# Optimization experiments

Hardware: AMD Instinct MI355X
Metric: run time of the kernel (lower is better)

The kernel has to match this reference:

```python
import jax, jax.numpy as jnp
import numpy as np
from jax import lax

NUM_CLASSES = 102
IN_CAPS = 2592
IN_DIM = 8
OUT_DIM = 16
ROUTINGS = 3
IMG = 112

def squash(s, axis=-1, eps=1e-8):
    sq = jnp.sum(s * s, axis=axis, keepdims=True)
    return (sq / (1.0 + sq)) * s / jnp.sqrt(sq + eps)

def conv2d(x, w, b, stride):
    y = lax.conv_general_dilated(x, w, (stride, stride), 'VALID',
                                 dimension_numbers=('NCHW', 'OIHW', 'NCHW'))
    return y + b[None, :, None, None]

def setup_inputs() -> dict:
    key = jax.random.key(0)
    ks = jax.random.split(key, 12)
    B = 32
    x = jax.random.normal(ks[0], (B, 3, IMG, IMG), jnp.float32)
    targets = jax.random.randint(ks[1], (B,), 0, NUM_CLASSES)
    conv1_w = jax.random.normal(ks[2], (256, 3, 11, 11), jnp.float32) * 0.02
    conv1_b = jnp.zeros((256,), jnp.float32)
    pc_w = jax.random.normal(ks[3], (256, 256, 9, 9), jnp.float32) * 0.02
    pc_b = jnp.zeros((256,), jnp.float32)
    W = jax.random.normal(ks[4], (NUM_CLASSES, IN_CAPS, OUT_DIM, IN_DIM), jnp.float32) * 0.01
    fc1_w = jax.random.normal(ks[5], (NUM_CLASSES * OUT_DIM, 512), jnp.float32) * 0.02
    fc1_b = jnp.zeros((512,), jnp.float32)
    fc2_w = jax.random.normal(ks[6], (512, 1024), jnp.float32) * 0.02
    fc2_b = jnp.zeros((1024,), jnp.float32)
    fc3_w = jax.random.normal(ks[7], (1024, 3 * IMG * IMG), jnp.float32) * 0.02
    fc3_b = jnp.zeros((3 * IMG * IMG,), jnp.float32)
    return dict(x=x, targets=targets, conv1_w=conv1_w, conv1_b=conv1_b,
                pc_w=pc_w, pc_b=pc_b, W=W,
                fc1_w=fc1_w, fc1_b=fc1_b, fc2_w=fc2_w, fc2_b=fc2_b,
                fc3_w=fc3_w, fc3_b=fc3_b)

def reference(x, targets, conv1_w, conv1_b, pc_w, pc_b, W,
              fc1_w, fc1_b, fc2_w, fc2_b, fc3_w, fc3_b):
    B = x.shape[0]
    # conv backbone: [B,3,112,112] -> [B,256,34,34]
    feat = jax.nn.relu(conv2d(x, conv1_w, conv1_b, 3))
    # primary caps conv: -> [B,256,9,9] -> [B,2592,8], squash
    pc = conv2d(feat, pc_w, pc_b, 3)
    u = squash(pc.reshape(B, IN_CAPS, IN_DIM))
    # prediction vectors: [B, O, N, D_out]
    x_hat = jnp.einsum('ondi,bni->bond', W, u)
    x_hat_sg = lax.stop_gradient(x_hat)
    b = jnp.zeros((B, NUM_CLASSES, IN_CAPS), x.dtype)
    v = None
    for it in range(ROUTINGS):
        c = jax.nn.softmax(b, axis=1)  # couple over out caps
        xh = x_hat if it == ROUTINGS - 1 else x_hat_sg
        s = jnp.einsum('bon,bond->bod', c, xh)
        v = squash(s)
        if it < ROUTINGS - 1:
            b = b + jnp.einsum('bond,bod->bon', xh, v)
    # reconstruction: mask by target class capsule
    mask = jax.nn.one_hot(targets, NUM_CLASSES, dtype=v.dtype)
    h = (v * mask[:, :, None]).reshape(B, NUM_CLASSES * OUT_DIM)
    h = jax.nn.relu(h @ fc1_w + fc1_b)
    h = jax.nn.relu(h @ fc2_w + fc2_b)
    recon = jax.nn.sigmoid(h @ fc3_w + fc3_b).reshape(B, 3, IMG, IMG)
    return (v, recon)
```

## Files before the change

### kernel.cpp

```cpp
#include <hip/hip_runtime.h>
#include <hip/hip_fp16.h>
#include <math.h>

#define B32   32
#define OCLS  102
#define NCAPS 2592

#define OFF_FEAT   0u
#define OFF_C1WT   10027008u
#define OFF_PCWQ   10076160u
#define OFF_PCP    11780096u
#define OFF_WQ2    17088512u
#define OFF_WQ     25555456u
#define OFF_U2     34022400u
#define OFF_CT     34685952u
#define OFF_DEN    38916096u
#define OFF_S      38999040u
#define OFF_V0     39051264u
#define OFF_V1     39103488u
#define OFF_VSQ    39155712u
#define OFF_H2T    39185152u
#define OFF_FC3P   39217920u

typedef __attribute__((ext_vector_type(8))) short short8;
typedef __attribute__((ext_vector_type(4))) float f32x4;
typedef long long i64;

__device__ __forceinline__ unsigned short f2b(float f) {
  union { float f; unsigned u; } v; v.f = f;
  unsigned r = v.u + 0x7fffu + ((v.u >> 16) & 1u);
  return (unsigned short)(r >> 16);
}

__device__ __forceinline__ float b2f(unsigned short h) {
  union { unsigned u; float f; } v; v.u = ((unsigned)h) << 16;
  return v.f;
}

__device__ __forceinline__ unsigned f2q_fast(float x) {
  union { float f; unsigned u; } v; v.f = x;
  unsigned s = (v.u >> 24) & 0x80u;
  unsigned au = v.u & 0x7fffffffu;
  if (au < 0x3c800000u) return s;
  if (au >= 0x43e00000u) return s | 0x7eu;
  unsigned r = au + 0x7ffffu + ((au >> 20) & 1u);
  unsigned e = (r >> 23) - 120u;
  unsigned m = (r >> 20) & 7u;
  return s | (e << 3) | m;
}

__device__ __forceinline__ unsigned fp8pair(float a, float b) {
#if __has_builtin(__builtin_amdgcn_cvt_pk_fp8_f32)
  return (unsigned)__builtin_amdgcn_cvt_pk_fp8_f32(a, b, 0, false) & 0xffffu;
#else
  return f2q_fast(a) | (f2q_fast(b) << 8);
#endif
}

__device__ __forceinline__ float rcpf(float x) {
#if __has_builtin(__builtin_amdgcn_rcpf)
  return __builtin_amdgcn_rcpf(x);
#else
  return 1.0f / x;
#endif
}

__global__ __launch_bounds__(256) void k_pack(const float* __restrict__ conv1_w,
                                              const float* __restrict__ pc_w,
                                              const float* __restrict__ W,
                                              unsigned short* __restrict__ C1WB,
                                              unsigned char* __restrict__ PCWQ,
                                              unsigned char* __restrict__ Wq2,
                                              unsigned char* __restrict__ Wq,
                                              float* __restrict__ S) {
  __shared__ unsigned char sq[64 * 128];
  int bb = blockIdx.x;
  int t = threadIdx.x;
  if (bb < 256) {
    if (t < 128) {
#pragma unroll
      for (int ci = 0; ci < 3; ++ci) {
        float v = (t < 121) ? conv1_w[bb * 363 + ci * 121 + t] : 0.f;
        C1WB[(ci * 256 + bb) * 128 + t] = f2b(v);
      }
    }
  } else if (bb < 512) {
    int co = bb - 256;
    for (int e = t; e < 20736; e += 256) {
      int ci = e / 81, tap = e - ci * 81;
      PCWQ[(size_t)ci * 26624 + co * 104 + tap] =
          (unsigned char)f2q_fast(pc_w[(size_t)co * 20736 + e] * 64.f);
    }
    for (int tap = 81; tap < 104; ++tap)
      PCWQ[(size_t)t * 26624 + co * 104 + tap] = 0;
  } else if (bb < 4643) {
    size_t base = (size_t)(bb - 512) * 8192;
    int g = t >> 3, seg = t & 7;
    int r0 = 2 * g, r1 = 2 * g + 1;
    const f32x4* s0 = (const f32x4*)(W + base + r0 * 128 + seg * 16);
    const f32x4* s1 = (const f32x4*)(W + base + r1 * 128 + seg * 16);
    f32x4 a0 = s0[0], a1 = s0[1], a2 = s0[2], a3 = s0[3];
    f32x4 c0 = s1[0], c1 = s1[1], c2 = s1[2], c3 = s1[3];
    asm volatile("" :: "v"(a0), "v"(a1), "v"(a2), "v"(a3),
                       "v"(c0), "v"(c1), "v"(c2), "v"(c3));
    unsigned w0[4], w1[4];
    f32x4 va[4] = {a0, a1, a2, a3}, vc[4] = {c0, c1, c2, c3};
#pragma unroll
    for (int j = 0; j < 4; ++j) {
      w0[j] = fp8pair(va[j][0] * 64.f, va[j][1] * 64.f) |
              (fp8pair(va[j][2] * 64.f, va[j][3] * 64.f) << 16);
      w1[j] = fp8pair(vc[j][0] * 64.f, vc[j][1] * 64.f) |
              (fp8pair(vc[j][2] * 64.f, vc[j][3] * 64.f) << 16);
    }
    *(uint4*)(Wq2 + base + r0 * 128 + seg * 16) = make_uint4(w0[0], w0[1], w0[2], w0[3]);
    *(uint4*)(Wq2 + base + r1 * 128 + seg * 16) = make_uint4(w1[0], w1[1], w1[2], w1[3]);
#pragma unroll
    for (int e = 0; e < 16; ++e) {
      int idx = seg * 16 + e, d = idx >> 3, i = idx & 7;
      sq[r0 * 128 + i * 16 + d] = (unsigned char)((w0[e >> 2] >> ((e & 3) * 8)) & 0xffu);
      sq[r1 * 128 + i * 16 + d] = (unsigned char)((w1[e >> 2] >> ((e & 3) * 8)) & 0xffu);
    }
    __syncthreads();
    *(uint4*)(Wq + base + (size_t)t * 16) = ((const uint4*)sq)[t];
    *(uint4*)(Wq + base + 4096 + (size_t)t * 16) = ((const uint4*)sq)[256 + t];
  } else {
    int idx = (bb - 4643) * 1024 + t * 4;
    *(float4*)(S + idx) = make_float4(0.f, 0.f, 0.f, 0.f);
  }
}

__global__ __launch_bounds__(256) void k_c1m(const float* __restrict__ x,
                                             const unsigned short* __restrict__ C1WB,
                                             const float* __restrict__ bias,
                                             unsigned short* __restrict__ feat2) {
  __shared__ unsigned short sh[48 * 128 + 128 * 128];
  unsigned short* lA = sh;
  unsigned short* lB = sh + 48 * 128;
  unsigned short* obuf = sh + 48 * 128;

  int bx = blockIdx.x;
  int hf = blockIdx.y;
  int b = bx / 34, ho = bx % 34;
  int t = threadIdx.x;
  int lane = t & 63, wv = t >> 6;
  int l15 = lane & 15, lh = lane >> 4;
  int rx = l15 & 7;

  {
    uint4 zz = make_uint4(0, 0, 0, 0);
    uint4* z = (uint4*)lA;
    for (int i = t; i < 48 * 128 / 8; i += 256) z[i] = zz;
  }
  __syncthreads();

  f32x4 acc[3][2];
#pragma unroll
  for (int mf = 0; mf < 3; ++mf)
#pragma unroll
    for (int nf = 0; nf < 2; ++nf) acc[mf][nf] = (f32x4){0.f, 0.f, 0.f, 0.f};

#pragma unroll 1
  for (int ci = 0; ci < 3; ++ci) {
    {
      const uint4* Bsrc = (const uint4*)(C1WB + ci * 32768 + hf * 16384);
#pragma unroll
      for (int i = 0; i < 8; ++i) {
        int f = i * 256 + t;
        int row = f >> 4, cu = f & 15;
        ((uint4*)lB)[row * 16 + (cu ^ (row & 7))] = Bsrc[f];
      }
    }
    for (int tk = t; tk < 374; tk += 256) {
      int kh = tk / 34, wo = tk - kh * 34;
      const float* src = x + ((size_t)(b * 3 + ci) * 112 + ho * 3 + kh) * 112 + wo * 3;
#pragma unroll
      for (int j = 0; j < 11; ++j) {
        int tap = kh * 11 + j;
        int cu = tap >> 3;
        lA[wo * 128 + (((cu ^ (wo & 7)) << 3) | (tap & 7))] = f2b(src[j]);
      }
    }
    __syncthreads();

#pragma unroll
    for (int s = 0; s < 4; ++s) {
      int cub = ((s * 4 + lh) ^ rx) << 3;
      short8 a0 = *(const short8*)(lA + (0 + l15) * 128 + cub);
      short8 a1 = *(const short8*)(lA + (16 + l15) * 128 + cub);
      short8 a2 = *(const short8*)(lA + (32 + l15) * 128 + cub);
      short8 b0 = *(const short8*)(lB + (wv * 32 + 0 + l15) * 128 + cub);
      short8 b1 = *(const short8*)(lB + (wv * 32 + 16 + l15) * 128 + cub);
      acc[0][0] = __builtin_amdgcn_mfma_f32_16x16x32_bf16(a0, b0, acc[0][0], 0, 0, 0);
      acc[0][1] = __builtin_amdgcn_mfma_f32_16x16x32_bf16(a0, b1, acc[0][1], 0, 0, 0);
      acc[1][0] = __builtin_amdgcn_mfma_f32_16x16x32_bf16(a1, b0, acc[1][0], 0, 0, 0);
      acc[1][1] = __builtin_amdgcn_mfma_f32_16x16x32_bf16(a1, b1, acc[1][1], 0, 0, 0);
      acc[2][0] = __builtin_amdgcn_mfma_f32_16x16x32_bf16(a2, b0, acc[2][0], 0, 0, 0);
      acc[2][1] = __builtin_amdgcn_mfma_f32_16x16x32_bf16(a2, b1, acc[2][1], 0, 0, 0);
    }
    __syncthreads();
  }

  float bv[2];
#pragma unroll
  for (int nf = 0; nf < 2; ++nf) bv[nf] = bias[hf * 128 + wv * 32 + nf * 16 + l15];
#pragma unroll
  for (int mf = 0; mf < 3; ++mf)
#pragma unroll
    for (int nf = 0; nf < 2; ++nf)
#pragma unroll
      for (int r = 0; r < 4; ++r) {
        int wo = mf * 16 + lh * 4 + r;
        if (wo < 36)
          obuf[(wv * 32 + nf * 16 + l15) * 36 + wo] =
              f2b(fmaxf(acc[mf][nf][r] + bv[nf], 0.f));
      }
  __syncthreads();
  uint4* dst = (uint4*)(feat2 + (size_t)bx * 9216 + hf * 4608);
  const uint4* srcb = (const uint4*)obuf;
  for (int i = t; i < 576; i += 256) dst[i] = srcb[i];
}

__device__ __forceinline__ void pc_gather8(const unsigned short* __restrict__ feat2,
                                           unsigned char* __restrict__ dstbuf,
                                           int mb, int ci, int t) {
  for (int task = t; task < 576; task += 256) {
    int m = task / 9, kh = task - m * 9;
    int gm = mb * 64 + m;
    if (gm < 2592) {
      int b = gm / 81, p = gm - b * 81;
      int ho = p / 9, wo = p - ho * 9;
      const unsigned short* src =
          feat2 + ((size_t)(b * 34 + ho * 3 + kh) * 256 + ci) * 36 + wo * 3;
      unsigned char* dst = dstbuf + m * 104 + kh * 9;
      unsigned p01 = fp8pair(b2f(src[0]), b2f(src[1]));
      unsigned p23 = fp8pair(b2f(src[2]), b2f(src[3]));
      unsigned p45 = fp8pair(b2f(src[4]), b2f(src[5]));
      unsigned p67 = fp8pair(b2f(src[6]), b2f(src[7]));
      unsigned p8  = fp8pair(b2f(src[8]), 0.f);
      dst[0] = p01; dst[1] = p01 >> 8;
      dst[2] = p23; dst[3] = p23 >> 8;
      dst[4] = p45; dst[5] = p45 >> 8;
      dst[6] = p67; dst[7] = p67 >> 8;
      dst[8] = p8;
    }
  }
}

__global__ __launch_bounds__(256, 3) void k_pc4(const unsigned short* __restrict__ feat2,
                                                const unsigned char* __restrict__ PCWQ,
                                                __half* __restrict__ pcp) {
  __shared__ unsigned char lA[2][64 * 104];

  int mb = blockIdx.x, kc = blockIdx.y;
  int t = threadIdx.x;
  int lane = t & 63, wv = t >> 6;
  int l15 = lane & 15, lh = lane >> 4;

  {
    uint4 zz = make_uint4(0, 0, 0, 0);
    uint4* z = (uint4*)lA;
    for (int i = t; i < 2 * 64 * 104 / 16; i += 256) z[i] = zz;
  }
  __syncthreads();
  pc_gather8(feat2, lA[0], mb, kc * 16, t);
  __syncthreads();

  f32x4 acc[4][4];
#pragma unroll
  for (int mf = 0; mf < 4; ++mf)
#pragma unroll
    for (int nf = 0; nf < 4; ++nf) acc[mf][nf] = (f32x4){0.f, 0.f, 0.f, 0.f};

#pragma unroll 1
  for (int cil = 0; cil < 16; ++cil) {
    int ci = kc * 16 + cil;
    int cur = cil & 1;

    i64 bfr[4][3];
    const unsigned char* Bbase = PCWQ + (size_t)ci * 26624 + (wv * 64 + l15) * 104 + lh * 8;
#pragma unroll
    for (int nf = 0; nf < 4; ++nf)
#pragma unroll
      for (int s = 0; s < 3; ++s)
        bfr[nf][s] = *(const i64*)(Bbase + nf * 16 * 104 + s * 32);

    if (cil < 15) pc_gather8(feat2, lA[cur ^ 1], mb, ci + 1, t);

    const unsigned char* arow = lA[cur] + l15 * 104 + lh * 8;
#pragma unroll
    for (int s = 0; s < 3; ++s) {
      i64 a0 = *(const i64*)(arow + s * 32);
      i64 a1 = *(const i64*)(arow + 16 * 104 + s * 32);
      i64 a2 = *(const i64*)(arow + 32 * 104 + s * 32);
      i64 a3 = *(const i64*)(arow + 48 * 104 + s * 32);
      acc[0][0] = __builtin_amdgcn_mfma_f32_16x16x32_fp8_fp8(a0, bfr[0][s], acc[0][0], 0, 0, 0);
      acc[0][1] = __builtin_amdgcn_mfma_f32_16x16x32_fp8_fp8(a0, bfr[1][s], acc[0][1], 0, 0, 0);
      acc[0][2] = __builtin_amdgcn_mfma_f32_16x16x32_fp8_fp8(a0, bfr[2][s], acc[0][2], 0, 0, 0);
      acc[0][3] = __builtin_amdgcn_mfma_f32_16x16x32_fp8_fp8(a0, bfr[3][s], acc[0][3], 0, 0, 0);
      acc[1][0] = __builtin_amdgcn_mfma_f32_16x16x32_fp8_fp8(a1, bfr[0][s], acc[1][0], 0, 0, 0);
      acc[1][1] = __builtin_amdgcn_mfma_f32_16x16x32_fp8_fp8(a1, bfr[1][s], acc[1][1], 0, 0, 0);
      acc[1][2] = __builtin_amdgcn_mfma_f32_16x16x32_fp8_fp8(a1, bfr[2][s], acc[1][2], 0, 0, 0);
      acc[1][3] = __builtin_amdgcn_mfma_f32_16x16x32_fp8_fp8(a1, bfr[3][s], acc[1][3], 0, 0, 0);
      acc[2][0] = __builtin_amdgcn_mfma_f32_16x16x32_fp8_fp8(a2, bfr[0][s], acc[2][0], 0, 0, 0);
      acc[2][1] = __builtin_amdgcn_mfma_f32_16x16x32_fp8_fp8(a2, bfr[1][s], acc[2][1], 0, 0, 0);
      acc[2][2] = __builtin_amdgcn_mfma_f32_16x16x32_fp8_fp8(a2, bfr[2][s], acc[2][2], 0, 0, 0);
      acc[2][3] = __builtin_amdgcn_mfma_f32_16x16x32_fp8_fp8(a2, bfr[3][s], acc[2][3], 0, 0, 0);
      acc[3][0] = __builtin_amdgcn_mfma_f32_16x16x32_fp8_fp8(a3, bfr[0][s], acc[3][0], 0, 0, 0);
      acc[3][1] = __builtin_amdgcn_mfma_f32_16x16x32_fp8_fp8(a3, bfr[1][s], acc[3][1], 0, 0, 0);
      acc[3][2] = __builtin_amdgcn_mfma_f32_16x16x32_fp8_fp8(a3, bfr[2][s], acc[3][2], 0, 0, 0);
      acc[3][3] = __builtin_amdgcn_mfma_f32_16x16x32_fp8_fp8(a3, bfr[3][s], acc[3][3], 0, 0, 0);
    }
    __syncthreads();
  }

#pragma unroll
  for (int mf = 0; mf < 4; ++mf) {
    int gm = mb * 64 + mf * 16 + lh * 4;
    if (gm < 2592) {
      __half* dst = pcp + (size_t)kc * 663552 + (size_t)gm * 256 + wv * 64 + l15;
#pragma unroll
      for (int nf = 0; nf < 4; ++nf)
#pragma unroll
        for (int r = 0; r < 4; ++r)
          dst[(size_t)r * 256 + nf * 16] = __float2half(acc[mf][nf][r]);
    }
  }
}

__global__ __launch_bounds__(256) void k_rs(const __half* __restrict__ pcp,
                                            const float* __restrict__ pcb,
                                            float* __restrict__ u2) {
  __shared__ float tile[81 * 17];
  int b = blockIdx.x;
  int cog = blockIdx.y;
  int c0 = cog * 16;
  int t = threadIdx.x;

  for (int e = t; e < 1296; e += 256) {
    int p = e >> 4, col = e & 15;
    const __half* base = pcp + (size_t)(b * 81 + p) * 256 + c0 + col;
    float s = 0.f;
#pragma unroll
    for (int c = 0; c < 16; ++c) s += __half2float(base[(size_t)c * 663552]);
    tile[p * 17 + col] = pcb[c0 + col] + s * 0.015625f;
  }
  __syncthreads();

  if (t < 162) {
    float v[8];
    float sq = 0.f;
#pragma unroll
    for (int i = 0; i < 8; ++i) {
      int g = t * 8 + i;
      int col = g / 81, p = g - col * 81;
      v[i] = tile[p * 17 + col];
      sq += v[i] * v[i];
    }
    float sc = (sq / (1.f + sq)) / sqrtf(sq + 1e-8f);
    int n = cog * 162 + t;
    float4* dst = (float4*)(u2 + ((size_t)b * 2592 + n) * 8);
    dst[0] = make_float4(v[0] * sc, v[1] * sc, v[2] * sc, v[3] * sc);
    dst[1] = make_float4(v[4] * sc, v[5] * sc, v[6] * sc, v[7] * sc);
  }
}

__global__ __launch_bounds__(128) void k_A3(const unsigned char* __restrict__ Wq,
                                            const float* __restrict__ u2,
                                            const unsigned char* __restrict__ vq,
                                            __half* __restrict__ cT,
                                            float* __restrict__ den) {
  int nb = blockIdx.x;
  int ch = blockIdx.y;
  int o0 = ch * 34;
  int t = threadIdx.x, wv = t >> 6, lane = t & 63;
  int l15 = lane & 15, g = lane >> 4;
  int n0 = nb * 4 + 2 * wv;
  int nl = g >> 1, ih = (g & 1) * 4;

  float4 u0 = *(const float4*)(u2 + (((size_t)l15 * 2592 + n0 + nl) * 8 + ih));
  float4 u1 = *(const float4*)(u2 + (((size_t)(l15 + 16) * 2592 + n0 + nl) * 8 + ih));

  int nlA = l15 >> 3, iA = l15 & 7;
  const unsigned char* Ap = Wq + (((size_t)(n0 + nlA)) * 8 + iA) * 16 + (g & 1) * 8 +
                            (size_t)o0 * 331776;
  const unsigned char* B0p = vq + (size_t)l15 * 16 + (g & 1) * 8 + (size_t)o0 * 512;
  bool act = (g < 2);

  float den0 = 0.f, den1 = 0.f;
#pragma unroll 2
  for (int oo = 0; oo < 34; ++oo) {
    i64 a = 0, b0 = 0, b1 = 0;
    if (act) {
      a  = *(const i64*)(Ap + (size_t)oo * 331776);
      b0 = *(const i64*)(B0p + (size_t)oo * 512);
      b1 = *(const i64*)(B0p + (size_t)oo * 512 + 256);
    }
    f32x4 d0 = {0.f, 0.f, 0.f, 0.f}, d1 = {0.f, 0.f, 0.f, 0.f};
    d0 = __builtin_amdgcn_mfma_f32_16x16x32_fp8_fp8(a, b0, d0, 0, 0, 0);
    d1 = __builtin_amdgcn_mfma_f32_16x16x32_fp8_fp8(a, b1, d1, 0, 0, 0);
    float p0 = d0[0] * u0.x + d0[1] * u0.y + d0[2] * u0.z + d0[3] * u0.w;
    float p1 = d1[0] * u1.x + d1[1] * u1.y + d1[2] * u1.z + d1[3] * u1.w;
    p0 += __shfl_xor(p0, 16);
    p1 += __shfl_xor(p1, 16);
    p0 *= 1.52587890625e-05f;
    p1 *= 1.52587890625e-05f;
    float e0 = __expf(p0), e1 = __expf(p1);
    den0 += e0; den1 += e1;
    if ((g & 1) == 0) {
      __half* dst = cT + ((size_t)(o0 + oo) * 2592 + n0 + nl) * 32 + l15;
      dst[0]  = __float2half(e0);
      dst[16] = __float2half(e1);
    }
  }
  if ((g & 1) == 0) {
    atomicAdd(den + (n0 + nl) * 32 + l15, den0);
    atomicAdd(den + (n0 + nl) * 32 + l15 + 16, den1);
  }
}

__device__ __forceinline__ i64 cu_pack8(float c, float4 a, float4 b) {
  union { unsigned u[2]; i64 v; } r;
  r.u[0] = fp8pair(c * a.x, c * a.y) | (fp8pair(c * a.z, c * a.w) << 16);
  r.u[1] = fp8pair(c * b.x, c * b.y) | (fp8pair(c * b.z, c * b.w) << 16);
  return r.v;
}

template <bool HASC>
__global__ __launch_bounds__(256) void k_B3(const unsigned char* __restrict__ Wq2,
                                            const float* __restrict__ u2,
                                            const __half* __restrict__ cT,
                                            const float* __restrict__ den,
                                            float* __restrict__ s) {
  int o = blockIdx.x, kc = blockIdx.y;
  int t = threadIdx.x, lane = t & 63, wv = t >> 6;
  int l15 = lane & 15, h = lane >> 4;

  f32x4 acc0 = {0.f, 0.f, 0.f, 0.f}, acc1 = {0.f, 0.f, 0.f, 0.f};

#pragma unroll 1
  for (int st = wv; st < 54; st += 4) {
    int n = kc * 216 + st * 4 + h;
    i64 aq = *(const i64*)(Wq2 + (((size_t)o * 2592 + n) * 16 + l15) * 8);

    const float4* u0p = (const float4*)(u2 + ((size_t)l15 * 2592 + n) * 8);
    float4 u0a = u0p[0], u0b = u0p[1];
    const float4* u1p = (const float4*)(u2 + ((size_t)(l15 + 16) * 2592 + n) * 8);
    float4 u1a = u1p[0], u1b = u1p[1];

    float c0 = 16.0f, c1 = 16.0f;
    if (HASC) {
      const __half* cp = cT + ((size_t)o * 2592 + n) * 32;
      float i0 = rcpf(den[n * 32 + l15]);
      float i1 = rcpf(den[n * 32 + l15 + 16]);
      c0 = 16.0f * __half2float(cp[l15]) * i0;
      c1 = 16.0f * __half2float(cp[l15 + 16]) * i1;
    }
    i64 b0 = cu_pack8(c0, u0a, u0b);
    i64 b1 = cu_pack8(c1, u1a, u1b);

    acc0 = __builtin_amdgcn_mfma_f32_16x16x32_fp8_fp8(aq, b0, acc0, 0, 0, 0);
    acc1 = __builtin_amdgcn_mfma_f32_16x16x32_fp8_fp8(aq, b1, acc1, 0, 0, 0);
  }

#pragma unroll
  for (int r = 0; r < 4; ++r) {
    atomicAdd(s + ((size_t)l15 * 102 + o) * 16 + h * 4 + r, acc0[r]);
    atomicAdd(s + ((size_t)(l15 + 16) * 102 + o) * 16 + h * 4 + r, acc1[r]);
  }
}

__global__ void k_R(const float* __restrict__ s, float scale,
                    float* __restrict__ vout, const float* __restrict__ addin,
                    unsigned char* __restrict__ vsq, float* __restrict__ szero,
                    float* __restrict__ dzero) {
  int t = blockIdx.x * 256 + threadIdx.x;
  if (dzero) {
    for (int i = t; i < 82944; i += 3328) dzero[i] = 0.f;
  }
  if (t >= 3264) return;
  const float* sp = s + t * 16;
  float r[16];
  float sq = 0.f;
#pragma unroll
  for (int d = 0; d < 16; ++d) {
    r[d] = sp[d] * scale;
    sq += r[d] * r[d];
  }
  if (szero) {
#pragma unroll
    for (int d = 0; d < 16; ++d) szero[t * 16 + d] = 0.f;
  }
  float sc = (sq / (1.f + sq)) / sqrtf(sq + 1e-8f);
  float vv[16];
#pragma unroll
  for (int d = 0; d < 16; ++d) {
    vv[d] = r[d] * sc;
    vout[t * 16 + d] = vv[d];
  }
  if (vsq) {
    int b = t / 102, o = t - b * 102;
    float w[16];
#pragma unroll
    for (int d = 0; d < 16; ++d)
      w[d] = (addin ? (addin[t * 16 + d] + vv[d]) : vv[d]) * 1024.f;
    unsigned words[4];
#pragma unroll
    for (int q = 0; q < 4; ++q)
      words[q] = fp8pair(w[4 * q], w[4 * q + 1]) | (fp8pair(w[4 * q + 2], w[4 * q + 3]) << 16);
    *(uint4*)(vsq + ((size_t)o * 32 + b) * 16) =
        make_uint4(words[0], words[1], words[2], words[3]);
  }
}

__global__ __launch_bounds__(512) void k_fc12(const float* __restrict__ v2,
                                              const int* __restrict__ tgt,
                                              const float* __restrict__ w1,
                                              const float* __restrict__ b1,
                                              const float* __restrict__ w2,
                                              const float* __restrict__ b2,
                                              float* __restrict__ h2T) {
  __shared__ float h1s[4][512];
  int bq = blockIdx.x;
  int t = threadIdx.x;
#pragma unroll
  for (int bi = 0; bi < 4; ++bi) {
    int b = bq * 4 + bi;
    int tb = tgt[b];
    float acc = b1[t];
    const float* vv = v2 + (b * 102 + tb) * 16;
    const float* wr = w1 + (tb * 16) * 512 + t;
#pragma unroll
    for (int d = 0; d < 16; ++d) acc += vv[d] * wr[d * 512];
    h1s[bi][t] = fmaxf(acc, 0.f);
  }
  __syncthreads();
  float a0[4], a1[4];
#pragma unroll
  for (int bi = 0; bi < 4; ++bi) { a0[bi] = b2[t]; a1[bi] = b2[t + 512]; }
  for (int k = 0; k < 512; ++k) {
    float w0 = w2[k * 1024 + t], w1v = w2[k * 1024 + t + 512];
#pragma unroll
    for (int bi = 0; bi < 4; ++bi) {
      float h = h1s[bi][k];
      a0[bi] += h * w0;
      a1[bi] += h * w1v;
    }
  }
  float4 o0, o1;
  o0.x = fmaxf(a0[0], 0.f); o0.y = fmaxf(a0[1], 0.f);
  o0.z = fmaxf(a0[2], 0.f); o0.w = fmaxf(a0[3], 0.f);
  o1.x = fmaxf(a1[0], 0.f); o1.y = fmaxf(a1[1], 0.f);
  o1.z = fmaxf(a1[2], 0.f); o1.w = fmaxf(a1[3], 0.f);
  *(float4*)(h2T + t * 32 + bq * 4) = o0;
  *(float4*)(h2T + (t + 512) * 32 + bq * 4) = o1;
}

__global__ void k_fc3a(const float* __restrict__ h2T, const float* __restrict__ w3,
                       float* __restrict__ p) {
  int j = blockIdx.x * 128 + threadIdx.x;
  int ky = blockIdx.y;
  float acc[32];
#pragma unroll
  for (int i = 0; i < 32; ++i) acc[i] = 0.f;
  int k0 = ky * 256;
  for (int k = k0; k < k0 + 256; ++k) {
    float wv = w3[(size_t)k * 37632 + j];
    const float4* hp = (const float4*)(h2T + k * 32);
#pragma unroll
    for (int q = 0; q < 8; ++q) {
      float4 h = hp[q];
      acc[q * 4 + 0] += h.x * wv; acc[q * 4 + 1] += h.y * wv;
      acc[q * 4 + 2] += h.z * wv; acc[q * 4 + 3] += h.w * wv;
    }
  }
#pragma unroll
  for (int i = 0; i < 32; ++i)
    p[((size_t)ky * 32 + i) * 37632 + j] = acc[i];
}

__global__ void k_fc3b(const float* __restrict__ p, const float* __restrict__ b3,
                       float* __restrict__ out) {
  int j = blockIdx.x * 256 + threadIdx.x;
  float bv = b3[j];
#pragma unroll 1
  for (int b = 0; b < 32; ++b) {
    float s = bv + p[(size_t)b * 37632 + j] + p[(size_t)(32 + b) * 37632 + j] +
              p[(size_t)(64 + b) * 37632 + j] + p[(size_t)(96 + b) * 37632 + j];
    out[52224 + (size_t)b * 37632 + j] = 1.0f / (1.0f + __expf(-s));
  }
}

extern "C" void kernel_launch(void* const* d_in, const int* in_sizes, int n_in,
                              void* d_out, int out_size, void* d_ws, size_t ws_size,
                              hipStream_t stream) {
  const float* x       = (const float*)d_in[0];
  const int*   targets = (const int*)d_in[1];
  const float* conv1_w = (const float*)d_in[2];
  const float* conv1_b = (const float*)d_in[3];
  const float* pc_w    = (const float*)d_in[4];
  const float* pc_b    = (const float*)d_in[5];
  const float* W       = (const float*)d_in[6];
  const float* fc1_w   = (const float*)d_in[7];
  const float* fc1_b   = (const float*)d_in[8];
  const float* fc2_w   = (const float*)d_in[9];
  const float* fc2_b   = (const float*)d_in[10];
  const float* fc3_w   = (const float*)d_in[11];
  const float* fc3_b   = (const float*)d_in[12];
  float* out = (float*)d_out;
  float* ws = (float*)d_ws;

  unsigned short* FEAT2 = (unsigned short*)(ws + OFF_FEAT);
  unsigned short* C1WB = (unsigned short*)(ws + OFF_C1WT);
  unsigned char* PCWQ = (unsigned char*)(ws + OFF_PCWQ);
  __half* PCP = (__half*)(ws + OFF_PCP);
  unsigned char* WQ2 = (unsigned char*)(ws + OFF_WQ2);
  unsigned char* WQ  = (unsigned char*)(ws + OFF_WQ);
  float* U2   = ws + OFF_U2;
  __half* CT  = (__half*)(ws + OFF_CT);
  float* DEN  = ws + OFF_DEN;
  float* S    = ws + OFF_S;
  float* V0   = ws + OFF_V0;
  float* V1   = ws + OFF_V1;
  unsigned char* VSQ = (unsigned char*)(ws + OFF_VSQ);
  float* H2T  = ws + OFF_H2T;
  float* FC3P = ws + OFF_FC3P;

  k_pack<<<dim3(4694), 256, 0, stream>>>(conv1_w, pc_w, W, C1WB, PCWQ, WQ2, WQ, S);

  k_c1m<<<dim3(1088, 2), 256, 0, stream>>>(x, C1WB, conv1_b, FEAT2);

  k_pc4<<<dim3(41, 16), 256, 0, stream>>>(FEAT2, PCWQ, PCP);
  k_rs<<<dim3(32, 16), 256, 0, stream>>>(PCP, pc_b, U2);

  k_B3<false><<<dim3(102, 12), 256, 0, stream>>>(WQ2, U2, nullptr, nullptr, S);
  k_R<<<dim3(13), 256, 0, stream>>>(S, 1.0f / (102.0f * 1024.0f), V0, nullptr, VSQ, S, DEN);

  k_A3<<<dim3(648, 3), 128, 0, stream>>>(WQ, U2, VSQ, CT, DEN);
  k_B3<true><<<dim3(102, 12), 256, 0, stream>>>(WQ2, U2, CT, DEN, S);
  k_R<<<dim3(13), 256, 0, stream>>>(S, 1.0f / 1024.0f, V1, V0, VSQ, S, DEN);

  k_A3<<<dim3(648, 3), 128, 0, stream>>>(WQ, U2, VSQ, CT, DEN);
  k_B3<true><<<dim3(102, 12), 256, 0, stream>>>(WQ2, U2, CT, DEN, S);
  k_R<<<dim3(13), 256, 0, stream>>>(S, 1.0f / 1024.0f, out, nullptr, nullptr, nullptr, nullptr);

  k_fc12<<<dim3(8), 512, 0, stream>>>(out, targets, fc1_w, fc1_b, fc2_w, fc2_b, H2T);
  k_fc3a<<<dim3(294, 4), 128, 0, stream>>>(H2T, fc3_w, FC3P);
  k_fc3b<<<dim3(147), 256, 0, stream>>>(FC3P, fc3_b, out);
}
```

Baseline: 549.2 us.

## Fold weight packing into conv kernels to overlap with compute

The standalone packing kernel is split up. Conv1 weight packing stays as a small kernel. Primary-caps weight packing becomes extra blocks of the conv1 kernel. Routing weight quantization and S zeroing become extra blocks of the primary-caps GEMM kernel. This lets memory-bound packing work run alongside compute-bound blocks instead of as a serial launch. In exchange, the packing blocks inherit the GEMM kernel's launch bounds and shared-memory footprint.

```diff
diff --git a/kernel.cpp b/kernel.cpp
--- a/kernel.cpp
+++ b/kernel.cpp
@@ -65,27 +65,29 @@
 #endif
 }
 
-__global__ __launch_bounds__(256) void k_pack(const float* __restrict__ conv1_w,
-                                              const float* __restrict__ pc_w,
-                                              const float* __restrict__ W,
-                                              unsigned short* __restrict__ C1WB,
-                                              unsigned char* __restrict__ PCWQ,
-                                              unsigned char* __restrict__ Wq2,
-                                              unsigned char* __restrict__ Wq,
-                                              float* __restrict__ S) {
-  __shared__ unsigned char sq[64 * 128];
+__global__ __launch_bounds__(128) void k_pack0(const float* __restrict__ conv1_w,
+                                               unsigned short* __restrict__ C1WB) {
+  int co = blockIdx.x;
+  int t = threadIdx.x;
+#pragma unroll
+  for (int ci = 0; ci < 3; ++ci) {
+    float v = (t < 121) ? conv1_w[co * 363 + ci * 121 + t] : 0.f;
+    C1WB[(ci * 256 + co) * 128 + t] = f2b(v);
+  }
+}
+
+__global__ __launch_bounds__(256) void k_c1m(const float* __restrict__ x,
+                                             const unsigned short* __restrict__ C1WB,
+                                             const float* __restrict__ bias,
+                                             unsigned short* __restrict__ feat2,
+                                             const float* __restrict__ pc_w,
+                                             unsigned char* __restrict__ PCWQ) {
+  __shared__ unsigned short sh[48 * 128 + 128 * 128];
   int bb = blockIdx.x;
   int t = threadIdx.x;
-  if (bb < 256) {
-    if (t < 128) {
-#pragma unroll
-      for (int ci = 0; ci < 3; ++ci) {
-        float v = (t < 121) ? conv1_w[bb * 363 + ci * 121 + t] : 0.f;
-        C1WB[(ci * 256 + bb) * 128 + t] = f2b(v);
-      }
-    }
-  } else if (bb < 512) {
-    int co = bb - 256;
+
+  if (bb >= 2176) {
+    int co = bb - 2176;
     for (int e = t; e < 20736; e += 256) {
       int ci = e / 81, tap = e - ci * 81;
       PCWQ[(size_t)ci * 26624 + co * 104 + tap] =
@@ -93,55 +95,16 @@
     }
     for (int tap = 81; tap < 104; ++tap)
       PCWQ[(size_t)t * 26624 + co * 104 + tap] = 0;
-  } else if (bb < 4643) {
-    size_t base = (size_t)(bb - 512) * 8192;
-    int g = t >> 3, seg = t & 7;
-    int r0 = 2 * g, r1 = 2 * g + 1;
-    const f32x4* s0 = (const f32x4*)(W + base + r0 * 128 + seg * 16);
-    const f32x4* s1 = (const f32x4*)(W + base + r1 * 128 + seg * 16);
-    f32x4 a0 = s0[0], a1 = s0[1], a2 = s0[2], a3 = s0[3];
-    f32x4 c0 = s1[0], c1 = s1[1], c2 = s1[2], c3 = s1[3];
-    asm volatile("" :: "v"(a0), "v"(a1), "v"(a2), "v"(a3),
-                       "v"(c0), "v"(c1), "v"(c2), "v"(c3));
-    unsigned w0[4], w1[4];
-    f32x4 va[4] = {a0, a1, a2, a3}, vc[4] = {c0, c1, c2, c3};
-#pragma unroll
-    for (int j = 0; j < 4; ++j) {
-      w0[j] = fp8pair(va[j][0] * 64.f, va[j][1] * 64.f) |
-              (fp8pair(va[j][2] * 64.f, va[j][3] * 64.f) << 16);
-      w1[j] = fp8pair(vc[j][0] * 64.f, vc[j][1] * 64.f) |
-              (fp8pair(vc[j][2] * 64.f, vc[j][3] * 64.f) << 16);
-    }
-    *(uint4*)(Wq2 + base + r0 * 128 + seg * 16) = make_uint4(w0[0], w0[1], w0[2], w0[3]);
-    *(uint4*)(Wq2 + base + r1 * 128 + seg * 16) = make_uint4(w1[0], w1[1], w1[2], w1[3]);
-#pragma unroll
-    for (int e = 0; e < 16; ++e) {
-      int idx = seg * 16 + e, d = idx >> 3, i = idx & 7;
-      sq[r0 * 128 + i * 16 + d] = (unsigned char)((w0[e >> 2] >> ((e & 3) * 8)) & 0xffu);
-      sq[r1 * 128 + i * 16 + d] = (unsigned char)((w1[e >> 2] >> ((e & 3) * 8)) & 0xffu);
-    }
-    __syncthreads();
-    *(uint4*)(Wq + base + (size_t)t * 16) = ((const uint4*)sq)[t];
-    *(uint4*)(Wq + base + 4096 + (size_t)t * 16) = ((const uint4*)sq)[256 + t];
-  } else {
-    int idx = (bb - 4643) * 1024 + t * 4;
-    *(float4*)(S + idx) = make_float4(0.f, 0.f, 0.f, 0.f);
-  }
-}
-
-__global__ __launch_bounds__(256) void k_c1m(const float* __restrict__ x,
-                                             const unsigned short* __restrict__ C1WB,
-                                             const float* __restrict__ bias,
-                                             unsigned short* __restrict__ feat2) {
-  __shared__ unsigned short sh[48 * 128 + 128 * 128];
+    return;
+  }
+
   unsigned short* lA = sh;
   unsigned short* lB = sh + 48 * 128;
   unsigned short* obuf = sh + 48 * 128;
 
-  int bx = blockIdx.x;
-  int hf = blockIdx.y;
+  int bx = bb >> 1;
+  int hf = bb & 1;
   int b = bx / 34, ho = bx % 34;
-  int t = threadIdx.x;
   int lane = t & 63, wv = t >> 6;
   int l15 = lane & 15, lh = lane >> 4;
   int rx = l15 & 7;
@@ -248,17 +211,60 @@
 
 __global__ __launch_bounds__(256, 3) void k_pc4(const unsigned short* __restrict__ feat2,
                                                 const unsigned char* __restrict__ PCWQ,
-                                                __half* __restrict__ pcp) {
-  __shared__ unsigned char lA[2][64 * 104];
-
-  int mb = blockIdx.x, kc = blockIdx.y;
+                                                __half* __restrict__ pcp,
+                                                const float* __restrict__ W,
+                                                unsigned char* __restrict__ Wq2,
+                                                unsigned char* __restrict__ Wq,
+                                                float* __restrict__ S) {
+  __shared__ unsigned char shmem[2 * 64 * 104];
+  int bb = blockIdx.x;
   int t = threadIdx.x;
+
+  if (bb >= 4787) {
+    int idx = (bb - 4787) * 1024 + t * 4;
+    *(float4*)(S + idx) = make_float4(0.f, 0.f, 0.f, 0.f);
+    return;
+  }
+  if (bb >= 656) {
+    unsigned char* sq = shmem;
+    size_t base = (size_t)(bb - 656) * 8192;
+    int g = t >> 3, seg = t & 7;
+    int r0 = 2 * g, r1 = 2 * g + 1;
+    const f32x4* s0 = (const f32x4*)(W + base + r0 * 128 + seg * 16);
+    const f32x4* s1 = (const f32x4*)(W + base + r1 * 128 + seg * 16);
+    f32x4 a0 = s0[0], a1 = s0[1], a2 = s0[2], a3 = s0[3];
+    f32x4 c0 = s1[0], c1 = s1[1], c2 = s1[2], c3 = s1[3];
+    unsigned w0[4], w1[4];
+    f32x4 va[4] = {a0, a1, a2, a3}, vc[4] = {c0, c1, c2, c3};
+#pragma unroll
+    for (int j = 0; j < 4; ++j) {
+      w0[j] = fp8pair(va[j][0] * 64.f, va[j][1] * 64.f) |
+              (fp8pair(va[j][2] * 64.f, va[j][3] * 64.f) << 16);
+      w1[j] = fp8pair(vc[j][0] * 64.f, vc[j][1] * 64.f) |
+              (fp8pair(vc[j][2] * 64.f, vc[j][3] * 64.f) << 16);
+    }
+    *(uint4*)(Wq2 + base + r0 * 128 + seg * 16) = make_uint4(w0[0], w0[1], w0[2], w0[3]);
+    *(uint4*)(Wq2 + base + r1 * 128 + seg * 16) = make_uint4(w1[0], w1[1], w1[2], w1[3]);
+#pragma unroll
+    for (int e = 0; e < 16; ++e) {
+      int idx = seg * 16 + e, d = idx >> 3, i = idx & 7;
+      sq[r0 * 128 + i * 16 + d] = (unsigned char)((w0[e >> 2] >> ((e & 3) * 8)) & 0xffu);
+      sq[r1 * 128 + i * 16 + d] = (unsigned char)((w1[e >> 2] >> ((e & 3) * 8)) & 0xffu);
+    }
+    __syncthreads();
+    *(uint4*)(Wq + base + (size_t)t * 16) = ((const uint4*)sq)[t];
+    *(uint4*)(Wq + base + 4096 + (size_t)t * 16) = ((const uint4*)sq)[256 + t];
+    return;
+  }
+
+  unsigned char (*lA)[64 * 104] = (unsigned char (*)[64 * 104])shmem;
+  int kc = bb & 15, mb = bb >> 4;
   int lane = t & 63, wv = t >> 6;
   int l15 = lane & 15, lh = lane >> 4;
 
   {
     uint4 zz = make_uint4(0, 0, 0, 0);
-    uint4* z = (uint4*)lA;
+    uint4* z = (uint4*)shmem;
     for (int i = t; i < 2 * 64 * 104 / 16; i += 256) z[i] = zz;
   }
   __syncthreads();
@@ -625,11 +631,11 @@
   float* H2T  = ws + OFF_H2T;
   float* FC3P = ws + OFF_FC3P;
 
-  k_pack<<<dim3(4694), 256, 0, stream>>>(conv1_w, pc_w, W, C1WB, PCWQ, WQ2, WQ, S);
-
-  k_c1m<<<dim3(1088, 2), 256, 0, stream>>>(x, C1WB, conv1_b, FEAT2);
-
-  k_pc4<<<dim3(41, 16), 256, 0, stream>>>(FEAT2, PCWQ, PCP);
+  k_pack0<<<dim3(256), 128, 0, stream>>>(conv1_w, C1WB);
+
+  k_c1m<<<dim3(2432), 256, 0, stream>>>(x, C1WB, conv1_b, FEAT2, pc_w, PCWQ);
+
+  k_pc4<<<dim3(4838), 256, 0, stream>>>(FEAT2, PCWQ, PCP, W, WQ2, WQ, S);
   k_rs<<<dim3(32, 16), 256, 0, stream>>>(PCP, pc_b, U2);
 
   k_B3<false><<<dim3(102, 12), 256, 0, stream>>>(WQ2, U2, nullptr, nullptr, S);
```

Measured after the change: 542.0 us (median of 2 runs). About the same (-1.3%).
